# Performance work log

Measured on AMD Instinct MI355X. Metric: run time of the kernel, lower is better.

The kernel has to match this reference:

```python
import jax, jax.numpy as jnp
import numpy as np

BN_EPS = 1e-5
N_NODES = 50000


def _bn(h, g, b, m, v):
    # BatchNorm1d in inference mode: running stats
    return (h - m) * (g / jnp.sqrt(v + BN_EPS)) + b


def _gin_agg(x, src, dst):
    # GINConv with eps=0: (1+eps)*x + sum_{j in N(i)} x_j
    agg = jax.ops.segment_sum(x[src], dst, num_segments=x.shape[0])
    return x + agg


def setup_inputs() -> dict:
    key = jax.random.key(0)
    ks = jax.random.split(key, 24)
    N, E, C_in, H, C_out = N_NODES, 800000, 128, 128, 64
    x = jax.random.normal(ks[0], (N, C_in), dtype=jnp.float32)
    edge_index = jax.random.randint(ks[1], (2, E), 0, N, dtype=jnp.int64)

    def lin(k, i, o):
        s = 1.0 / np.sqrt(i)
        return jax.random.uniform(k, (i, o), jnp.float32, -s, s)

    def bnp(k, d):
        k1, k2 = jax.random.split(k)
        return (jnp.ones((d,), jnp.float32), jnp.zeros((d,), jnp.float32),
                jax.random.normal(k1, (d,), jnp.float32) * 0.1,
                jax.random.uniform(k2, (d,), jnp.float32, 0.5, 1.5))
    g0, be0, m0, v0 = bnp(ks[4], H)
    g1, be1, m1, v1 = bnp(ks[5], H)
    g2, be2, m2, v2 = bnp(ks[6], H)
    return {
        "x": x, "edge_index": edge_index,
        "W0": lin(ks[7], C_in, H), "b0": jnp.zeros((H,), jnp.float32),
        "g0": g0, "be0": be0, "m0": m0, "v0": v0,
        "W1": lin(ks[8], H, H), "b1": jnp.zeros((H,), jnp.float32),
        "g1": g1, "be1": be1, "m1": m1, "v1": v1,
        "W2": lin(ks[9], H, H), "b2": jnp.zeros((H,), jnp.float32),
        "g2": g2, "be2": be2, "m2": m2, "v2": v2,
        "W3": lin(ks[10], H, C_out), "b3": jnp.zeros((C_out,), jnp.float32),
    }


def reference(x, edge_index, W0, b0, g0, be0, m0, v0,
              W1, b1, g1, be1, m1, v1,
              W2, b2, g2, be2, m2, v2, W3, b3):
    src, dst = edge_index[0], edge_index[1]
    # layer 0: GINConv(firstmlp) -> relu (dropout identity in eval)
    h = _gin_agg(x, src, dst)
    h = jax.nn.relu(_bn(h @ W0 + b0, g0, be0, m0, v0))  # firstmlp
    h = jax.nn.relu(h)
    # layer 1: GINConv(mlp) -> relu
    h = _gin_agg(h, src, dst)
    h = jax.nn.relu(_bn(h @ W1 + b1, g1, be1, m1, v1))  # mlp
    h = jax.nn.relu(h)
    # layer 2: GINConv(lastmlp); if_auc=True -> raw output
    h = _gin_agg(h, src, dst)
    h = jax.nn.relu(_bn(h @ W2 + b2, g2, be2, m2, v2))
    out = h @ W3 + b3
    return out
```

## Files before the change

kernel.cpp:

```cpp
#include <hip/hip_runtime.h>

#define HDIM 128
#define NBMAX 512

typedef __attribute__((ext_vector_type(8))) short short8;
typedef __attribute__((ext_vector_type(4))) float f32x4;

__device__ __forceinline__ short f2bf(float f) {
    union { float f; unsigned u; } x; x.f = f;
    unsigned r = x.u + 0x7FFF + ((x.u >> 16) & 1);
    return (short)(r >> 16);
}
__device__ __forceinline__ float bf2f(short s) {
    union { unsigned u; float f; } x;
    x.u = ((unsigned)(unsigned short)s) << 16;
    return x.f;
}

__global__ void cvt_bf16(short* __restrict__ dst, const float* __restrict__ src, int n) {
    int i = (blockIdx.x * blockDim.x + threadIdx.x) * 4;
    int stride = gridDim.x * blockDim.x * 4;
    for (; i < n; i += stride) {
        float4 v = *(const float4*)(src + i);
        short4 o;
        o.x = f2bf(v.x); o.y = f2bf(v.y); o.z = f2bf(v.z); o.w = f2bf(v.w);
        *(short4*)(dst + i) = o;
    }
}

__global__ void hist_buckets(int* __restrict__ ghist, const int* __restrict__ dsti, int E, int NB) {
    __shared__ int h[NBMAX];
    for (int b = threadIdx.x; b < NBMAX; b += 256) h[b] = 0;
    __syncthreads();
    int e = blockIdx.x * blockDim.x + threadIdx.x;
    int stride = gridDim.x * blockDim.x;
    for (; e < E; e += stride) atomicAdd(&h[dsti[e] >> 7], 1);
    __syncthreads();
    for (int b = threadIdx.x; b < NB; b += 256) { int c = h[b]; if (c) atomicAdd(&ghist[b], c); }
}

__global__ void scan_buckets(int* __restrict__ bucketPtr, int* __restrict__ bucketCur,
                             const int* __restrict__ ghist, int NB,
                             int* __restrict__ rowptr, int N, int E) {
    int lane = threadIdx.x;
    int carry = 0;
    int nch = (NB + 63) / 64;
    for (int s = 0; s < nch; s++) {
        int idx = s * 64 + lane;
        int c = idx < NB ? ghist[idx] : 0;
        int inc = c;
        #pragma unroll
        for (int st = 1; st < 64; st <<= 1) { int n = __shfl_up(inc, st, 64); if (lane >= st) inc += n; }
        int exc = inc - c + carry;
        if (idx < NB) { bucketPtr[idx] = exc; bucketCur[idx] = exc; }
        carry += __shfl(inc, 63, 64);
    }
    if (lane == 0) { bucketPtr[NB] = carry; rowptr[N] = E; }
}

__global__ __launch_bounds__(256) void scatter_recs(int* __restrict__ recs, int* __restrict__ bucketCur,
                                                    const int* __restrict__ srci, const int* __restrict__ dsti,
                                                    int E, int NB) {
    __shared__ int hist[NBMAX];
    __shared__ int gb[NBMAX];
    const int t = threadIdx.x;
    const int base = blockIdx.x * 4096;
    for (int b = t; b < NBMAX; b += 256) hist[b] = 0;
    __syncthreads();
    #pragma unroll
    for (int i = 0; i < 16; i++) {
        int e = base + i * 256 + t;
        if (e < E) atomicAdd(&hist[dsti[e] >> 7], 1);
    }
    __syncthreads();
    for (int b = t; b < NB; b += 256) {
        int c = hist[b];
        gb[b] = c ? atomicAdd(&bucketCur[b], c) : 0;
        hist[b] = 0;
    }
    __syncthreads();
    #pragma unroll
    for (int i = 0; i < 16; i++) {
        int e = base + i * 256 + t;
        if (e < E) {
            int d = dsti[e], s = srci[e];
            int b = d >> 7;
            int off = atomicAdd(&hist[b], 1);
            recs[gb[b] + off] = ((d & 127) << 16) | s;
        }
    }
}

__global__ __launch_bounds__(256) void build_csr_local(
        unsigned short* __restrict__ csrH, int* __restrict__ rowptr,
        const int* __restrict__ recs, const int* __restrict__ bucketPtr, int N) {
    const int b = blockIdx.x;
    const int base = bucketPtr[b];
    const int cnt  = bucketPtr[b + 1] - base;
    __shared__ int nh[128];
    __shared__ int cur[128];
    const int t = threadIdx.x;
    if (t < 128) nh[t] = 0;
    __syncthreads();
    for (int i = t; i < cnt; i += 256) atomicAdd(&nh[recs[base + i] >> 16], 1);
    __syncthreads();
    if (t < 64) {
        int lane = t;
        int c0 = nh[lane], c1 = nh[64 + lane];
        int i0 = c0;
        #pragma unroll
        for (int s = 1; s < 64; s <<= 1) { int n = __shfl_up(i0, s, 64); if (lane >= s) i0 += n; }
        int tot0 = __shfl(i0, 63, 64);
        int i1 = c1;
        #pragma unroll
        for (int s = 1; s < 64; s <<= 1) { int n = __shfl_up(i1, s, 64); if (lane >= s) i1 += n; }
        i1 += tot0;
        int e0 = i0 - c0, e1 = i1 - c1;
        cur[lane] = e0; cur[64 + lane] = e1;
        int idx0 = b * 128 + lane, idx1 = b * 128 + 64 + lane;
        if (idx0 <= N) rowptr[idx0] = base + e0;
        if (idx1 <= N) rowptr[idx1] = base + e1;
    }
    __syncthreads();
    for (int i = t; i < cnt; i += 256) {
        int r = recs[base + i];
        int off = atomicAdd(&cur[r >> 16], 1);
        csrH[base + off] = (unsigned short)(r & 0xffff);
    }
}

__global__ void prep_all(short* __restrict__ Wp0, short* __restrict__ Wp1,
                         short* __restrict__ Wp2, short* __restrict__ Wp3,
                         const float* __restrict__ W0, const float* __restrict__ W1,
                         const float* __restrict__ W2, const float* __restrict__ W3,
                         float* __restrict__ scbuf, int* __restrict__ ghist,
                         const float* __restrict__ b0, const float* __restrict__ g0,
                         const float* __restrict__ be0, const float* __restrict__ m0,
                         const float* __restrict__ v0,
                         const float* __restrict__ b1, const float* __restrict__ g1,
                         const float* __restrict__ be1, const float* __restrict__ m1,
                         const float* __restrict__ v1,
                         const float* __restrict__ b2, const float* __restrict__ g2,
                         const float* __restrict__ be2, const float* __restrict__ m2,
                         const float* __restrict__ v2,
                         const float* __restrict__ b3) {
    int bid = blockIdx.x;
    if (bid < 24) {
        int layer = bid >> 3;
        int tid = (bid & 7) * 256 + threadIdx.x;
        const float* W = layer == 0 ? W0 : layer == 1 ? W1 : W2;
        short* Wp = layer == 0 ? Wp0 : layer == 1 ? Wp1 : Wp2;
        int lane = tid & 63;
        int ks = (tid >> 6) & 3;
        int nt = tid >> 8;
        int n = nt * 16 + (lane & 15);
        int k0 = ks * 32 + ((lane >> 4) & 3) * 8;
        short8 v;
        #pragma unroll
        for (int j = 0; j < 8; j++) v[j] = f2bf(W[(long)(k0 + j) * HDIM + n]);
        ((short8*)Wp)[tid] = v;
    } else if (bid < 28) {
        int tid = (bid - 24) * 256 + threadIdx.x;
        int lane = tid & 63;
        int ks = (tid >> 6) & 3;
        int nt = tid >> 8;
        int n = nt * 16 + (lane & 15);
        int k0 = ks * 32 + ((lane >> 4) & 3) * 8;
        short8 v;
        #pragma unroll
        for (int j = 0; j < 8; j++) v[j] = f2bf(W3[(long)(k0 + j) * 64 + n]);
        ((short8*)Wp3)[tid] = v;
    } else if (bid == 28) {
        for (int iter = 0; iter < 2; iter++) {
            int slot = iter * 256 + threadIdx.x;
            if (slot < 128) {
                int c = slot;
                float s = g0[c] * rsqrtf(v0[c] + 1e-5f);
                scbuf[c] = s;
                scbuf[128 + c] = (b0[c] - m0[c]) * s + be0[c];
            } else if (slot < 256) {
                int c = slot - 128;
                float s = g1[c] * rsqrtf(v1[c] + 1e-5f);
                scbuf[256 + c] = s;
                scbuf[256 + 128 + c] = (b1[c] - m1[c]) * s + be1[c];
            } else if (slot < 384) {
                int c = slot - 256;
                float s = g2[c] * rsqrtf(v2[c] + 1e-5f);
                scbuf[512 + c] = s;
                scbuf[512 + 128 + c] = (b2[c] - m2[c]) * s + be2[c];
            } else if (slot < 448) {
                int c = slot - 384;
                scbuf[768 + c] = 1.f;
                scbuf[768 + 128 + c] = b3[c];
            }
        }
    } else {
        ghist[threadIdx.x] = 0;
        ghist[256 + threadIdx.x] = 0;
    }
}

template<bool FINAL>
__global__ __launch_bounds__(256) void gin_layer(
        short* __restrict__ outb, float* __restrict__ outf,
        const short* __restrict__ xp,
        const int* __restrict__ rowptr, const unsigned short* __restrict__ csrH,
        const short* __restrict__ Wp,
        const float* __restrict__ scale, const float* __restrict__ offset,
        const short* __restrict__ Wp2,
        const float* __restrict__ scale2, const float* __restrict__ offset2,
        int N) {
    __shared__ short As[16 * HDIM];
    const int t = threadIdx.x;
    const int row0 = blockIdx.x * 16;

    {
        const short8* xp8 = (const short8*)xp;
        int rl = t >> 4;
        int chunk = t & 15;
        int node = row0 + rl;
        float facc[8];
        if (node < N) {
            short8 id = xp8[(long)node * 16 + chunk];
            #pragma unroll
            for (int j = 0; j < 8; j++) facc[j] = bf2f(id[j]);
            int s0 = rowptr[node], s1 = rowptr[node + 1];
            int deg = s1 - s0;
            const unsigned short* nb = csrH + s0;
            int k = 0;
            for (; k + 4 <= deg; k += 4) {
                int n0 = nb[k], n1 = nb[k + 1], n2 = nb[k + 2], n3 = nb[k + 3];
                short8 v0 = xp8[(long)n0 * 16 + chunk];
                short8 v1 = xp8[(long)n1 * 16 + chunk];
                short8 v2 = xp8[(long)n2 * 16 + chunk];
                short8 v3 = xp8[(long)n3 * 16 + chunk];
                #pragma unroll
                for (int j = 0; j < 8; j++)
                    facc[j] += (bf2f(v0[j]) + bf2f(v1[j])) + (bf2f(v2[j]) + bf2f(v3[j]));
            }
            for (; k < deg; k++) {
                short8 v0 = xp8[(long)nb[k] * 16 + chunk];
                #pragma unroll
                for (int j = 0; j < 8; j++) facc[j] += bf2f(v0[j]);
            }
        } else {
            #pragma unroll
            for (int j = 0; j < 8; j++) facc[j] = 0.f;
        }
        short8 o;
        #pragma unroll
        for (int j = 0; j < 8; j++) o[j] = f2bf(facc[j]);
        int baddr = (rl * 256 + chunk * 16) ^ ((rl & 7) << 4);
        *(short8*)((char*)As + baddr) = o;
    }
    __syncthreads();

    const int lane = t & 63, w = t >> 6;
    const int rl0 = lane & 15;
    const int hi = (lane >> 4) & 3;
    short8 a[4];
    #pragma unroll
    for (int ks = 0; ks < 4; ks++) {
        int baddr = (rl0 * 256 + ks * 64 + hi * 16) ^ ((rl0 & 7) << 4);
        a[ks] = *(const short8*)((const char*)As + baddr);
    }
    if (FINAL) __syncthreads();

    const short8* bp = (const short8*)Wp + lane;
    const int c = lane & 15;
    const int rb = hi * 4;

    #pragma unroll
    for (int i = 0; i < 2; i++) {
        int nt = w * 2 + i;
        f32x4 acc = {0.f, 0.f, 0.f, 0.f};
        short8 b0 = bp[(nt * 4 + 0) * 64];
        short8 b1 = bp[(nt * 4 + 1) * 64];
        short8 b2 = bp[(nt * 4 + 2) * 64];
        short8 b3 = bp[(nt * 4 + 3) * 64];
        acc = __builtin_amdgcn_mfma_f32_16x16x32_bf16(a[0], b0, acc, 0, 0, 0);
        acc = __builtin_amdgcn_mfma_f32_16x16x32_bf16(a[1], b1, acc, 0, 0, 0);
        acc = __builtin_amdgcn_mfma_f32_16x16x32_bf16(a[2], b2, acc, 0, 0, 0);
        acc = __builtin_amdgcn_mfma_f32_16x16x32_bf16(a[3], b3, acc, 0, 0, 0);
        int cc = nt * 16 + c;
        float s = scale[cc], o = offset[cc];
        if (!FINAL) {
            #pragma unroll
            for (int r = 0; r < 4; r++) {
                int rr = row0 + rb + r;
                if (rr < N) {
                    float val = fmaxf(acc[r] * s + o, 0.f);
                    outb[(long)rr * HDIM + cc] = f2bf(val);
                }
            }
        } else {
            #pragma unroll
            for (int r = 0; r < 4; r++) {
                int rloc = rb + r;
                float val = fmaxf(acc[r] * s + o, 0.f);
                int baddr = (rloc * 256 + cc * 2) ^ ((rloc & 7) << 4);
                *(short*)((char*)As + baddr) = f2bf(val);
            }
        }
    }

    if (FINAL) {
        __syncthreads();
        short8 a2[4];
        #pragma unroll
        for (int ks = 0; ks < 4; ks++) {
            int baddr = (rl0 * 256 + ks * 64 + hi * 16) ^ ((rl0 & 7) << 4);
            a2[ks] = *(const short8*)((const char*)As + baddr);
        }
        const short8* bp2 = (const short8*)Wp2 + lane;
        int nt = w;
        f32x4 acc = {0.f, 0.f, 0.f, 0.f};
        short8 b0 = bp2[(nt * 4 + 0) * 64];
        short8 b1 = bp2[(nt * 4 + 1) * 64];
        short8 b2 = bp2[(nt * 4 + 2) * 64];
        short8 b3v = bp2[(nt * 4 + 3) * 64];
        acc = __builtin_amdgcn_mfma_f32_16x16x32_bf16(a2[0], b0, acc, 0, 0, 0);
        acc = __builtin_amdgcn_mfma_f32_16x16x32_bf16(a2[1], b1, acc, 0, 0, 0);
        acc = __builtin_amdgcn_mfma_f32_16x16x32_bf16(a2[2], b2, acc, 0, 0, 0);
        acc = __builtin_amdgcn_mfma_f32_16x16x32_bf16(a2[3], b3v, acc, 0, 0, 0);
        int cc = nt * 16 + c;
        float s2 = scale2[cc], o2 = offset2[cc];
        #pragma unroll
        for (int r = 0; r < 4; r++) {
            int rr = row0 + rb + r;
            if (rr < N) outf[(long)rr * 64 + cc] = acc[r] * s2 + o2;
        }
    }
}

extern "C" void kernel_launch(void* const* d_in, const int* in_sizes, int n_in,
                              void* d_out, int out_size, void* d_ws, size_t ws_size,
                              hipStream_t stream) {
    const float* x  = (const float*)d_in[0];
    const int*   ei = (const int*)d_in[1];
    const int E = in_sizes[1] / 2;
    const int* srci = ei;
    const int* dsti = ei + E;

    const float* W0 = (const float*)d_in[2];
    const float* b0 = (const float*)d_in[3];
    const float* g0 = (const float*)d_in[4];
    const float* be0 = (const float*)d_in[5];
    const float* m0 = (const float*)d_in[6];
    const float* v0 = (const float*)d_in[7];
    const float* W1 = (const float*)d_in[8];
    const float* b1 = (const float*)d_in[9];
    const float* g1 = (const float*)d_in[10];
    const float* be1 = (const float*)d_in[11];
    const float* m1 = (const float*)d_in[12];
    const float* v1 = (const float*)d_in[13];
    const float* W2 = (const float*)d_in[14];
    const float* b2 = (const float*)d_in[15];
    const float* g2 = (const float*)d_in[16];
    const float* be2 = (const float*)d_in[17];
    const float* m2 = (const float*)d_in[18];
    const float* v2 = (const float*)d_in[19];
    const float* W3 = (const float*)d_in[20];
    const float* b3 = (const float*)d_in[21];

    const int N = in_sizes[0] / HDIM;
    const int NB = (N + 127) >> 7;
    float* out = (float*)d_out;

    short* ba = (short*)d_ws;
    short* bb = ba + (size_t)N * HDIM;
    int* rowptr = (int*)(bb + (size_t)N * HDIM);
    int* recs   = rowptr + ((N + 2 + 3) & ~3);
    unsigned short* csrH = (unsigned short*)(recs + E);
    int* ghist = (int*)(((uintptr_t)(csrH + E) + 63) & ~(uintptr_t)63);
    int* bucketPtr = ghist + NBMAX;
    int* bucketCur = bucketPtr + NBMAX + 4;
    short* Wp0 = (short*)(((uintptr_t)(bucketCur + NBMAX) + 63) & ~(uintptr_t)63);
    short* Wp1  = Wp0 + 16384;
    short* Wp2  = Wp1 + 16384;
    short* Wp3  = Wp2 + 16384;
    float* scbuf = (float*)(Wp3 + 8192);

    const int layerBlocks = (N + 15) / 16;
    const int nElem = N * HDIM;
    int cvtBlocks = (nElem / 4 + 255) / 256; if (cvtBlocks > 2048) cvtBlocks = 2048;

    prep_all<<<30, 256, 0, stream>>>(Wp0, Wp1, Wp2, Wp3, W0, W1, W2, W3, scbuf, ghist,
                                     b0, g0, be0, m0, v0,
                                     b1, g1, be1, m1, v1,
                                     b2, g2, be2, m2, v2, b3);
    cvt_bf16<<<cvtBlocks, 256, 0, stream>>>(ba, x, nElem);
    hist_buckets<<<256, 256, 0, stream>>>(ghist, dsti, E, NB);
    scan_buckets<<<1, 64, 0, stream>>>(bucketPtr, bucketCur, ghist, NB, rowptr, N, E);
    scatter_recs<<<(E + 4095) / 4096, 256, 0, stream>>>(recs, bucketCur, srci, dsti, E, NB);
    build_csr_local<<<NB, 256, 0, stream>>>(csrH, rowptr, recs, bucketPtr, N);

    gin_layer<false><<<layerBlocks, 256, 0, stream>>>(
        bb, nullptr, ba, rowptr, csrH, Wp0, scbuf + 0, scbuf + 128,
        nullptr, nullptr, nullptr, N);
    gin_layer<false><<<layerBlocks, 256, 0, stream>>>(
        ba, nullptr, bb, rowptr, csrH, Wp1, scbuf + 256, scbuf + 384,
        nullptr, nullptr, nullptr, N);
    gin_layer<true><<<layerBlocks, 256, 0, stream>>>(
        nullptr, out, ba, rowptr, csrH, Wp2, scbuf + 512, scbuf + 640,
        Wp3, scbuf + 768, scbuf + 896, N);
}
```

Baseline: 160.3 us.

## Fuse bf16 convert, histogram and scan into one kernel; unroll gather by eight

Merges the feature conversion, the destination-bucket histogram and the bucket scan into a single launch. The last histogram block, detected with an atomic counter, performs the scan, which removes two kernel launches and their serialization gaps. The neighbor-gather loop in the GIN layers is also unrolled from 4 to 8 with a 2-wide tail, putting more loads in flight per thread. This adds a counter reset in prep and a threadfence-based last-block protocol, and the wider unroll may raise register pressure.

```diff
diff --git a/kernel.cpp b/kernel.cpp
--- a/kernel.cpp
+++ b/kernel.cpp
@@ -17,45 +17,55 @@
     return x.f;
 }
 
-__global__ void cvt_bf16(short* __restrict__ dst, const float* __restrict__ src, int n) {
-    int i = (blockIdx.x * blockDim.x + threadIdx.x) * 4;
-    int stride = gridDim.x * blockDim.x * 4;
-    for (; i < n; i += stride) {
-        float4 v = *(const float4*)(src + i);
-        short4 o;
-        o.x = f2bf(v.x); o.y = f2bf(v.y); o.z = f2bf(v.z); o.w = f2bf(v.w);
-        *(short4*)(dst + i) = o;
-    }
-}
-
-__global__ void hist_buckets(int* __restrict__ ghist, const int* __restrict__ dsti, int E, int NB) {
+__global__ __launch_bounds__(256) void cvt_hist_scan(
+        short* __restrict__ dst, const float* __restrict__ src, int n,
+        int* __restrict__ ghist, const int* __restrict__ dsti, int E, int NB,
+        int cvtB, int histB, int* __restrict__ done,
+        int* __restrict__ bucketPtr, int* __restrict__ bucketCur,
+        int* __restrict__ rowptr, int N) {
+    const int t = threadIdx.x;
+    if (blockIdx.x < cvtB) {
+        int i = (blockIdx.x * 256 + t) * 4;
+        int stride = cvtB * 256 * 4;
+        for (; i < n; i += stride) {
+            float4 v = *(const float4*)(src + i);
+            short4 o;
+            o.x = f2bf(v.x); o.y = f2bf(v.y); o.z = f2bf(v.z); o.w = f2bf(v.w);
+            *(short4*)(dst + i) = o;
+        }
+        return;
+    }
     __shared__ int h[NBMAX];
-    for (int b = threadIdx.x; b < NBMAX; b += 256) h[b] = 0;
-    __syncthreads();
-    int e = blockIdx.x * blockDim.x + threadIdx.x;
-    int stride = gridDim.x * blockDim.x;
+    __shared__ int amLast;
+    const int hb = blockIdx.x - cvtB;
+    for (int b = t; b < NBMAX; b += 256) h[b] = 0;
+    __syncthreads();
+    int e = hb * 256 + t;
+    int stride = histB * 256;
     for (; e < E; e += stride) atomicAdd(&h[dsti[e] >> 7], 1);
     __syncthreads();
-    for (int b = threadIdx.x; b < NB; b += 256) { int c = h[b]; if (c) atomicAdd(&ghist[b], c); }
-}
-
-__global__ void scan_buckets(int* __restrict__ bucketPtr, int* __restrict__ bucketCur,
-                             const int* __restrict__ ghist, int NB,
-                             int* __restrict__ rowptr, int N, int E) {
-    int lane = threadIdx.x;
-    int carry = 0;
-    int nch = (NB + 63) / 64;
-    for (int s = 0; s < nch; s++) {
-        int idx = s * 64 + lane;
-        int c = idx < NB ? ghist[idx] : 0;
-        int inc = c;
-        #pragma unroll
-        for (int st = 1; st < 64; st <<= 1) { int n = __shfl_up(inc, st, 64); if (lane >= st) inc += n; }
-        int exc = inc - c + carry;
-        if (idx < NB) { bucketPtr[idx] = exc; bucketCur[idx] = exc; }
-        carry += __shfl(inc, 63, 64);
-    }
-    if (lane == 0) { bucketPtr[NB] = carry; rowptr[N] = E; }
+    for (int b = t; b < NB; b += 256) { int c = h[b]; if (c) atomicAdd(&ghist[b], c); }
+    __threadfence();
+    if (t == 0) amLast = (atomicAdd(done, 1) == histB - 1);
+    __syncthreads();
+    if (!amLast) return;
+    __threadfence();
+    if (t < 64) {
+        int lane = t;
+        int carry = 0;
+        int nch = (NB + 63) / 64;
+        for (int s = 0; s < nch; s++) {
+            int idx = s * 64 + lane;
+            int c = idx < NB ? ghist[idx] : 0;
+            int inc = c;
+            #pragma unroll
+            for (int st = 1; st < 64; st <<= 1) { int nn = __shfl_up(inc, st, 64); if (lane >= st) inc += nn; }
+            int exc = inc - c + carry;
+            if (idx < NB) { bucketPtr[idx] = exc; bucketCur[idx] = exc; }
+            carry += __shfl(inc, 63, 64);
+        }
+        if (lane == 0) { bucketPtr[NB] = carry; rowptr[N] = E; }
+    }
 }
 
 __global__ __launch_bounds__(256) void scatter_recs(int* __restrict__ recs, int* __restrict__ bucketCur,
@@ -133,7 +143,7 @@
                          short* __restrict__ Wp2, short* __restrict__ Wp3,
                          const float* __restrict__ W0, const float* __restrict__ W1,
                          const float* __restrict__ W2, const float* __restrict__ W3,
-                         float* __restrict__ scbuf, int* __restrict__ ghist,
+                         float* __restrict__ scbuf, int* __restrict__ ghist, int* __restrict__ done,
                          const float* __restrict__ b0, const float* __restrict__ g0,
                          const float* __restrict__ be0, const float* __restrict__ m0,
                          const float* __restrict__ v0,
@@ -197,6 +207,7 @@
     } else {
         ghist[threadIdx.x] = 0;
         ghist[256 + threadIdx.x] = 0;
+        if (threadIdx.x == 0) *done = 0;
     }
 }
 
@@ -228,17 +239,30 @@
             int deg = s1 - s0;
             const unsigned short* nb = csrH + s0;
             int k = 0;
-            for (; k + 4 <= deg; k += 4) {
+            for (; k + 8 <= deg; k += 8) {
                 int n0 = nb[k], n1 = nb[k + 1], n2 = nb[k + 2], n3 = nb[k + 3];
+                int n4 = nb[k + 4], n5 = nb[k + 5], n6 = nb[k + 6], n7 = nb[k + 7];
                 short8 v0 = xp8[(long)n0 * 16 + chunk];
                 short8 v1 = xp8[(long)n1 * 16 + chunk];
                 short8 v2 = xp8[(long)n2 * 16 + chunk];
                 short8 v3 = xp8[(long)n3 * 16 + chunk];
+                short8 v4 = xp8[(long)n4 * 16 + chunk];
+                short8 v5 = xp8[(long)n5 * 16 + chunk];
+                short8 v6 = xp8[(long)n6 * 16 + chunk];
+                short8 v7 = xp8[(long)n7 * 16 + chunk];
                 #pragma unroll
                 for (int j = 0; j < 8; j++)
-                    facc[j] += (bf2f(v0[j]) + bf2f(v1[j])) + (bf2f(v2[j]) + bf2f(v3[j]));
-            }
-            for (; k < deg; k++) {
+                    facc[j] += ((bf2f(v0[j]) + bf2f(v1[j])) + (bf2f(v2[j]) + bf2f(v3[j])))
+                             + ((bf2f(v4[j]) + bf2f(v5[j])) + (bf2f(v6[j]) + bf2f(v7[j])));
+            }
+            for (; k + 2 <= deg; k += 2) {
+                int n0 = nb[k], n1 = nb[k + 1];
+                short8 v0 = xp8[(long)n0 * 16 + chunk];
+                short8 v1 = xp8[(long)n1 * 16 + chunk];
+                #pragma unroll
+                for (int j = 0; j < 8; j++) facc[j] += bf2f(v0[j]) + bf2f(v1[j]);
+            }
+            if (k < deg) {
                 short8 v0 = xp8[(long)nb[k] * 16 + chunk];
                 #pragma unroll
                 for (int j = 0; j < 8; j++) facc[j] += bf2f(v0[j]);
@@ -375,7 +399,8 @@
     int* ghist = (int*)(((uintptr_t)(csrH + E) + 63) & ~(uintptr_t)63);
     int* bucketPtr = ghist + NBMAX;
     int* bucketCur = bucketPtr + NBMAX + 4;
-    short* Wp0 = (short*)(((uintptr_t)(bucketCur + NBMAX) + 63) & ~(uintptr_t)63);
+    int* done      = bucketCur + NBMAX;
+    short* Wp0 = (short*)(((uintptr_t)(done + 4) + 63) & ~(uintptr_t)63);
     short* Wp1  = Wp0 + 16384;
     short* Wp2  = Wp1 + 16384;
     short* Wp3  = Wp2 + 16384;
@@ -383,15 +408,16 @@
 
     const int layerBlocks = (N + 15) / 16;
     const int nElem = N * HDIM;
-    int cvtBlocks = (nElem / 4 + 255) / 256; if (cvtBlocks > 2048) cvtBlocks = 2048;
-
-    prep_all<<<30, 256, 0, stream>>>(Wp0, Wp1, Wp2, Wp3, W0, W1, W2, W3, scbuf, ghist,
+    int cvtB = (nElem / 4 + 255) / 256; if (cvtB > 2048) cvtB = 2048;
+    const int histB = 256;
+
+    prep_all<<<30, 256, 0, stream>>>(Wp0, Wp1, Wp2, Wp3, W0, W1, W2, W3, scbuf, ghist, done,
                                      b0, g0, be0, m0, v0,
                                      b1, g1, be1, m1, v1,
                                      b2, g2, be2, m2, v2, b3);
-    cvt_bf16<<<cvtBlocks, 256, 0, stream>>>(ba, x, nElem);
-    hist_buckets<<<256, 256, 0, stream>>>(ghist, dsti, E, NB);
-    scan_buckets<<<1, 64, 0, stream>>>(bucketPtr, bucketCur, ghist, NB, rowptr, N, E);
+    cvt_hist_scan<<<cvtB + histB, 256, 0, stream>>>(ba, x, nElem, ghist, dsti, E, NB,
+                                                    cvtB, histB, done,
+                                                    bucketPtr, bucketCur, rowptr, N);
     scatter_recs<<<(E + 4095) / 4096, 256, 0, stream>>>(recs, bucketCur, srci, dsti, E, NB);
     build_csr_local<<<NB, 256, 0, stream>>>(csrH, rowptr, recs, bucketPtr, N);
 
```

Result: slower. 173.1 us (+8.0%).
